# Kernel optimization log

Hardware: AMD Instinct MI355X
Metric: run time of the kernel (lower is better)

Reference implementation:

```python
import jax, jax.numpy as jnp
import numpy as np

SCALE = 64.0
MARGIN = 0.35
EPS = 1e-12  # torch F.normalize eps


def _l2norm(a, axis):
    n = jnp.sqrt(jnp.sum(a * a, axis=axis, keepdims=True))
    return a / jnp.maximum(n, EPS)


def setup_inputs() -> dict:
    key = jax.random.key(0)
    k1, k2, k3 = jax.random.split(key, 3)
    B, D, C = 512, 512, 100000
    x = jax.random.normal(k1, (B, D), dtype=jnp.float32)
    gt = jax.random.randint(k2, (B,), 0, C, dtype=jnp.int64)
    # kaiming_normal_ on [C, D]: std = sqrt(2 / fan_in) with fan_in = D
    wt = jax.random.normal(k3, (C, D), dtype=jnp.float32) * np.sqrt(2.0 / D)
    return {"x": x, "gt": gt, "wt": wt}


def reference(x, gt, wt):
    wt_norm = _l2norm(wt, axis=1)          # [C, D]
    x_norm = _l2norm(x, axis=1)            # [B, D]
    cos = jnp.einsum("bd,cd->bc", x_norm, wt_norm)  # [B, C]
    # margin only at target index (avoids materializing one-hot)
    b = jnp.arange(x.shape[0])
    margin_score = cos.at[b, gt].add(-MARGIN)
    logits = SCALE * margin_score
    logp = jax.nn.log_softmax(logits, axis=-1)
    nll = -logp[b, gt]
    return jnp.mean(nll)
```

## Files before the change

### kernel.cpp

```cpp
#include <hip/hip_runtime.h>
#include <hip/hip_bf16.h>

#define DIM 512
#define BATCH 512
#define CCLS 100000
#define BN 128
#define NT 782

typedef __attribute__((ext_vector_type(4))) float f32x4;

__device__ __forceinline__ void async_copy16(const unsigned char* g, unsigned char* l) {
  __builtin_amdgcn_global_load_lds((const __attribute__((address_space(1))) void*)g,
                                   (__attribute__((address_space(3))) void*)l, 16, 0, 0);
}

__global__ __launch_bounds__(256) void xquant(const float* __restrict__ x,
                                              unsigned char* __restrict__ xq,
                                              float* __restrict__ nx) {
  int wave = threadIdx.x >> 6;
  int lane = threadIdx.x & 63;
  int row = blockIdx.x * 4 + wave;
  const float4* src = (const float4*)(x + (size_t)row * DIM);
  float4 v0 = src[2 * lane];
  float4 v1 = src[2 * lane + 1];
  float ss = v0.x*v0.x + v0.y*v0.y + v0.z*v0.z + v0.w*v0.w
           + v1.x*v1.x + v1.y*v1.y + v1.z*v1.z + v1.w*v1.w;
  #pragma unroll
  for (int off = 32; off > 0; off >>= 1) ss += __shfl_xor(ss, off, 64);
  int p0 = __builtin_amdgcn_cvt_pk_fp8_f32(v0.x, v0.y, 0, false);
  p0     = __builtin_amdgcn_cvt_pk_fp8_f32(v0.z, v0.w, p0, true);
  int p1 = __builtin_amdgcn_cvt_pk_fp8_f32(v1.x, v1.y, 0, false);
  p1     = __builtin_amdgcn_cvt_pk_fp8_f32(v1.z, v1.w, p1, true);
  ((int2*)(xq + (size_t)row * DIM))[lane] = make_int2(p0, p1);
  if (lane == 0) nx[row] = fmaxf(sqrtf(ss), 1e-12f);
}

__global__ __launch_bounds__(1024) void cosface_fused(
    const unsigned char* __restrict__ xq,
    const float* __restrict__ wt,
    const int* __restrict__ gt,
    const float* __restrict__ nx,
    float* __restrict__ partial,
    float* __restrict__ tgt) {
  __shared__ __align__(16) unsigned char lds_a[512 * 128];
  __shared__ __align__(16) unsigned char lds_b[BN * 128];
  __shared__ float lds_rowsum[BATCH];
  __shared__ float lds_nx[BATCH];
  __shared__ float lds_nw[BN];
  __shared__ int lds_gt[BATCH];

  const int tid = threadIdx.x;
  const int lane = tid & 63;
  const int w = tid >> 6;
  const int wm = w >> 2;
  const int wn_ = w & 3;
  const int nt = blockIdx.x;

  if (tid < BATCH) {
    lds_rowsum[tid] = 0.f;
    lds_gt[tid] = gt[tid];
    lds_nx[tid] = nx[tid];
  }
  if (tid < BN) lds_nw[tid] = 0.f;

  unsigned int oa[4];
  #pragma unroll
  for (int j = 0; j < 4; ++j) {
    int c = j * 1024 + tid;
    int m = c >> 3;
    int qg = (c & 7) ^ (m & 7);
    oa[j] = (unsigned int)m * DIM + qg * 16;
  }
  const int mB = tid >> 3;
  const int qgB = (tid & 7) ^ (mB & 7);
  int rowB = nt * BN + mB;
  if (rowB >= CCLS) rowB = CCLS - 1;
  const float* wsrc = wt + (size_t)rowB * DIM + qgB * 16;

  f32x4 acc[8][2];
  #pragma unroll
  for (int i = 0; i < 8; ++i)
    #pragma unroll
    for (int j = 0; j < 2; ++j)
      acc[i][j] = (f32x4){0.f, 0.f, 0.f, 0.f};

  const int quad = lane >> 4;
  const int l15 = lane & 15;
  const int sw = l15 & 7;
  __syncthreads();

  for (int kk = 0; kk < 4; ++kk) {
    #pragma unroll
    for (int j = 0; j < 4; ++j)
      async_copy16(xq + oa[j] + kk * 128, &lds_a[(j * 1024 + w * 64) * 16]);
    {
      const float* p = wsrc + kk * 128;
      float4 f0 = *(const float4*)(p);
      float4 f1 = *(const float4*)(p + 4);
      float4 f2 = *(const float4*)(p + 8);
      float4 f3 = *(const float4*)(p + 12);
      f0.x*=16.f; f0.y*=16.f; f0.z*=16.f; f0.w*=16.f;
      f1.x*=16.f; f1.y*=16.f; f1.z*=16.f; f1.w*=16.f;
      f2.x*=16.f; f2.y*=16.f; f2.z*=16.f; f2.w*=16.f;
      f3.x*=16.f; f3.y*=16.f; f3.z*=16.f; f3.w*=16.f;
      float ss = f0.x*f0.x + f0.y*f0.y + f0.z*f0.z + f0.w*f0.w
               + f1.x*f1.x + f1.y*f1.y + f1.z*f1.z + f1.w*f1.w
               + f2.x*f2.x + f2.y*f2.y + f2.z*f2.z + f2.w*f2.w
               + f3.x*f3.x + f3.y*f3.y + f3.z*f3.z + f3.w*f3.w;
      int p0 = __builtin_amdgcn_cvt_pk_fp8_f32(f0.x, f0.y, 0, false);
      p0     = __builtin_amdgcn_cvt_pk_fp8_f32(f0.z, f0.w, p0, true);
      int p1 = __builtin_amdgcn_cvt_pk_fp8_f32(f1.x, f1.y, 0, false);
      p1     = __builtin_amdgcn_cvt_pk_fp8_f32(f1.z, f1.w, p1, true);
      int p2 = __builtin_amdgcn_cvt_pk_fp8_f32(f2.x, f2.y, 0, false);
      p2     = __builtin_amdgcn_cvt_pk_fp8_f32(f2.z, f2.w, p2, true);
      int p3 = __builtin_amdgcn_cvt_pk_fp8_f32(f3.x, f3.y, 0, false);
      p3     = __builtin_amdgcn_cvt_pk_fp8_f32(f3.z, f3.w, p3, true);
      ((int4*)lds_b)[tid] = make_int4(p0, p1, p2, p3);
      ss += __shfl_xor(ss, 1, 64);
      ss += __shfl_xor(ss, 2, 64);
      ss += __shfl_xor(ss, 4, 64);
      if ((lane & 7) == 0) atomicAdd(&lds_nw[mB], ss);
    }
    __syncthreads();

    #pragma unroll
    for (int s = 0; s < 4; ++s) {
      int g = s * 4 + quad;
      int cs = g >> 1;
      int h = (g & 1) * 8;
      long long af[8], bf[2];
      #pragma unroll
      for (int i = 0; i < 8; ++i)
        af[i] = *(const long long*)&lds_a[(wm * 128 + i * 16 + l15) * 128 + ((cs ^ sw) * 16) + h];
      #pragma unroll
      for (int j = 0; j < 2; ++j)
        bf[j] = *(const long long*)&lds_b[(wn_ * 32 + j * 16 + l15) * 128 + ((cs ^ sw) * 16) + h];
      #pragma unroll
      for (int i = 0; i < 8; ++i)
        #pragma unroll
        for (int j = 0; j < 2; ++j)
          acc[i][j] = __builtin_amdgcn_mfma_f32_16x16x32_fp8_fp8(af[i], bf[j], acc[i][j], 0, 0, 0);
    }
    __syncthreads();
  }

  float rnw[2];
  #pragma unroll
  for (int j = 0; j < 2; ++j)
    rnw[j] = 1.0f / fmaxf(sqrtf(lds_nw[wn_ * 32 + j * 16 + l15]), 1e-12f);
  #pragma unroll
  for (int i = 0; i < 8; ++i) {
    #pragma unroll
    for (int reg = 0; reg < 4; ++reg) {
      int m_loc = wm * 128 + i * 16 + quad * 4 + reg;
      int gtm = lds_gt[m_loc];
      float rx = 64.0f / lds_nx[m_loc];
      float s = 0.f;
      #pragma unroll
      for (int j = 0; j < 2; ++j) {
        int n_g = nt * BN + wn_ * 32 + j * 16 + l15;
        float logit = acc[i][j][reg] * rnw[j] * rx;
        if (n_g == gtm) {
          logit -= 64.f * 0.35f;
          tgt[m_loc] = logit;
        }
        if (n_g < CCLS) s += __expf(logit - 64.f);
      }
      #pragma unroll
      for (int off = 1; off < 16; off <<= 1) s += __shfl_xor(s, off, 64);
      if (l15 == 0) atomicAdd(&lds_rowsum[m_loc], s);
    }
  }
  __syncthreads();
  if (tid < BATCH)
    partial[(size_t)tid * NT + nt] = lds_rowsum[tid];
}

__global__ __launch_bounds__(64) void nll_rows(const float* __restrict__ partial,
                                               const float* __restrict__ tgt,
                                               float* __restrict__ nll) {
  int m = blockIdx.x;
  int lane = threadIdx.x;
  const float* row = partial + (size_t)m * NT;
  float s = 0.f;
  for (int t = lane; t < NT; t += 64) s += row[t];
  #pragma unroll
  for (int off = 32; off > 0; off >>= 1) s += __shfl_xor(s, off, 64);
  if (lane == 0) nll[m] = (logf(s) + 64.f) - tgt[m];
}

__global__ __launch_bounds__(512) void reduce_mean(const float* __restrict__ nll,
                                                   float* __restrict__ out) {
  __shared__ float red[BATCH];
  int m = threadIdx.x;
  red[m] = nll[m];
  __syncthreads();
  for (int k = 256; k > 0; k >>= 1) {
    if (m < k) red[m] += red[m + k];
    __syncthreads();
  }
  if (m == 0) out[0] = red[0] * (1.0f / BATCH);
}

extern "C" void kernel_launch(void* const* d_in, const int* in_sizes, int n_in,
                              void* d_out, int out_size, void* d_ws, size_t ws_size,
                              hipStream_t stream) {
  const float* x  = (const float*)d_in[0];
  const int*   gt = (const int*)d_in[1];
  const float* wt = (const float*)d_in[2];
  float* out = (float*)d_out;

  char* ws = (char*)d_ws;
  unsigned char* xq = (unsigned char*)ws;
  float* nx         = (float*)(ws + 262144);
  float* partial    = (float*)(ws + 264192);
  float* tgt        = (float*)(ws + 1865728);
  float* nll        = (float*)(ws + 1867776);

  xquant<<<BATCH / 4, 256, 0, stream>>>(x, xq, nx);
  cosface_fused<<<NT, 1024, 0, stream>>>(xq, wt, gt, nx, partial, tgt);
  nll_rows<<<BATCH, 64, 0, stream>>>(partial, tgt, nll);
  reduce_mean<<<1, BATCH, 0, stream>>>(nll, out);
}
```

Measured before the change: 393.7 us.

## Split GEMM tile into 256x64 blocks with XCD-aware mapping and weight prefetch

```diff
diff --git a/kernel.cpp b/kernel.cpp
--- a/kernel.cpp
+++ b/kernel.cpp
@@ -4,8 +4,9 @@
 #define DIM 512
 #define BATCH 512
 #define CCLS 100000
-#define BN 128
-#define NT 782
+#define BM 256
+#define BN 64
+#define NT 1563
 
 typedef __attribute__((ext_vector_type(4))) float f32x4;
 
@@ -35,41 +36,47 @@
   if (lane == 0) nx[row] = fmaxf(sqrtf(ss), 1e-12f);
 }
 
-__global__ __launch_bounds__(1024) void cosface_fused(
+__global__ __launch_bounds__(512, 4) void cosface_fused(
     const unsigned char* __restrict__ xq,
     const float* __restrict__ wt,
     const int* __restrict__ gt,
     const float* __restrict__ nx,
     float* __restrict__ partial,
     float* __restrict__ tgt) {
-  __shared__ __align__(16) unsigned char lds_a[512 * 128];
+  __shared__ __align__(16) unsigned char lds_a[BM * 128];
   __shared__ __align__(16) unsigned char lds_b[BN * 128];
-  __shared__ float lds_rowsum[BATCH];
-  __shared__ float lds_nx[BATCH];
+  __shared__ float lds_rowsum[BM];
+  __shared__ float lds_nx[BM];
   __shared__ float lds_nw[BN];
-  __shared__ int lds_gt[BATCH];
+  __shared__ int lds_gt[BM];
 
   const int tid = threadIdx.x;
   const int lane = tid & 63;
   const int w = tid >> 6;
-  const int wm = w >> 2;
-  const int wn_ = w & 3;
-  const int nt = blockIdx.x;
-
-  if (tid < BATCH) {
+  const int wm = w >> 1;
+  const int wn_ = w & 1;
+
+  int flat = blockIdx.x;
+  int xcd = flat & 7;
+  int idx = flat >> 3;
+  int f = ((xcd < 6) ? xcd * 391 : (6 * 391 + (xcd - 6) * 390)) + idx;
+  const int mt = f & 1;
+  const int nt = f >> 1;
+
+  if (tid < BM) {
     lds_rowsum[tid] = 0.f;
-    lds_gt[tid] = gt[tid];
-    lds_nx[tid] = nx[tid];
+    lds_gt[tid] = gt[mt * BM + tid];
+    lds_nx[tid] = nx[mt * BM + tid];
   }
   if (tid < BN) lds_nw[tid] = 0.f;
 
   unsigned int oa[4];
   #pragma unroll
   for (int j = 0; j < 4; ++j) {
-    int c = j * 1024 + tid;
+    int c = j * 512 + tid;
     int m = c >> 3;
     int qg = (c & 7) ^ (m & 7);
-    oa[j] = (unsigned int)m * DIM + qg * 16;
+    oa[j] = (unsigned int)(mt * BM + m) * DIM + qg * 16;
   }
   const int mB = tid >> 3;
   const int qgB = (tid & 7) ^ (mB & 7);
@@ -77,9 +84,9 @@
   if (rowB >= CCLS) rowB = CCLS - 1;
   const float* wsrc = wt + (size_t)rowB * DIM + qgB * 16;
 
-  f32x4 acc[8][2];
-  #pragma unroll
-  for (int i = 0; i < 8; ++i)
+  f32x4 acc[4][2];
+  #pragma unroll
+  for (int i = 0; i < 4; ++i)
     #pragma unroll
     for (int j = 0; j < 2; ++j)
       acc[i][j] = (f32x4){0.f, 0.f, 0.f, 0.f};
@@ -87,59 +94,91 @@
   const int quad = lane >> 4;
   const int l15 = lane & 15;
   const int sw = l15 & 7;
+
+  int p0, p1, p2, p3;
+  float ssq;
+  {
+    float4 f0 = *(const float4*)(wsrc);
+    float4 f1 = *(const float4*)(wsrc + 4);
+    float4 f2 = *(const float4*)(wsrc + 8);
+    float4 f3 = *(const float4*)(wsrc + 12);
+    f0.x*=16.f; f0.y*=16.f; f0.z*=16.f; f0.w*=16.f;
+    f1.x*=16.f; f1.y*=16.f; f1.z*=16.f; f1.w*=16.f;
+    f2.x*=16.f; f2.y*=16.f; f2.z*=16.f; f2.w*=16.f;
+    f3.x*=16.f; f3.y*=16.f; f3.z*=16.f; f3.w*=16.f;
+    ssq = f0.x*f0.x + f0.y*f0.y + f0.z*f0.z + f0.w*f0.w
+        + f1.x*f1.x + f1.y*f1.y + f1.z*f1.z + f1.w*f1.w
+        + f2.x*f2.x + f2.y*f2.y + f2.z*f2.z + f2.w*f2.w
+        + f3.x*f3.x + f3.y*f3.y + f3.z*f3.z + f3.w*f3.w;
+    p0 = __builtin_amdgcn_cvt_pk_fp8_f32(f0.x, f0.y, 0, false);
+    p0 = __builtin_amdgcn_cvt_pk_fp8_f32(f0.z, f0.w, p0, true);
+    p1 = __builtin_amdgcn_cvt_pk_fp8_f32(f1.x, f1.y, 0, false);
+    p1 = __builtin_amdgcn_cvt_pk_fp8_f32(f1.z, f1.w, p1, true);
+    p2 = __builtin_amdgcn_cvt_pk_fp8_f32(f2.x, f2.y, 0, false);
+    p2 = __builtin_amdgcn_cvt_pk_fp8_f32(f2.z, f2.w, p2, true);
+    p3 = __builtin_amdgcn_cvt_pk_fp8_f32(f3.x, f3.y, 0, false);
+    p3 = __builtin_amdgcn_cvt_pk_fp8_f32(f3.z, f3.w, p3, true);
+  }
   __syncthreads();
 
   for (int kk = 0; kk < 4; ++kk) {
+    ((int4*)lds_b)[tid] = make_int4(p0, p1, p2, p3);
     #pragma unroll
     for (int j = 0; j < 4; ++j)
-      async_copy16(xq + oa[j] + kk * 128, &lds_a[(j * 1024 + w * 64) * 16]);
+      async_copy16(xq + oa[j] + kk * 128, &lds_a[(j * 512 + w * 64) * 16]);
     {
-      const float* p = wsrc + kk * 128;
-      float4 f0 = *(const float4*)(p);
-      float4 f1 = *(const float4*)(p + 4);
-      float4 f2 = *(const float4*)(p + 8);
-      float4 f3 = *(const float4*)(p + 12);
+      float s = ssq;
+      s += __shfl_xor(s, 1, 64);
+      s += __shfl_xor(s, 2, 64);
+      s += __shfl_xor(s, 4, 64);
+      if ((lane & 7) == 0) atomicAdd(&lds_nw[mB], s);
+    }
+    __syncthreads();
+
+    float4 f0, f1, f2, f3;
+    if (kk < 3) {
+      const float* p = wsrc + (kk + 1) * 128;
+      f0 = *(const float4*)(p);
+      f1 = *(const float4*)(p + 4);
+      f2 = *(const float4*)(p + 8);
+      f3 = *(const float4*)(p + 12);
+    }
+    #pragma unroll
+    for (int s = 0; s < 4; ++s) {
+      int g = s * 4 + quad;
+      int cs = g >> 1;
+      int h = (g & 1) * 8;
+      long long af[4], bf[2];
+      #pragma unroll
+      for (int i = 0; i < 4; ++i)
+        af[i] = *(const long long*)&lds_a[(wm * 64 + i * 16 + l15) * 128 + ((cs ^ sw) * 16) + h];
+      #pragma unroll
+      for (int j = 0; j < 2; ++j)
+        bf[j] = *(const long long*)&lds_b[(wn_ * 32 + j * 16 + l15) * 128 + ((cs ^ sw) * 16) + h];
+      #pragma unroll
+      for (int i = 0; i < 4; ++i)
+        #pragma unroll
+        for (int j = 0; j < 2; ++j)
+          acc[i][j] = __builtin_amdgcn_mfma_f32_16x16x32_fp8_fp8(af[i], bf[j], acc[i][j], 0, 0, 0);
+    }
+
+    if (kk < 3) {
       f0.x*=16.f; f0.y*=16.f; f0.z*=16.f; f0.w*=16.f;
       f1.x*=16.f; f1.y*=16.f; f1.z*=16.f; f1.w*=16.f;
       f2.x*=16.f; f2.y*=16.f; f2.z*=16.f; f2.w*=16.f;
       f3.x*=16.f; f3.y*=16.f; f3.z*=16.f; f3.w*=16.f;
-      float ss = f0.x*f0.x + f0.y*f0.y + f0.z*f0.z + f0.w*f0.w
-               + f1.x*f1.x + f1.y*f1.y + f1.z*f1.z + f1.w*f1.w
-               + f2.x*f2.x + f2.y*f2.y + f2.z*f2.z + f2.w*f2.w
-               + f3.x*f3.x + f3.y*f3.y + f3.z*f3.z + f3.w*f3.w;
-      int p0 = __builtin_amdgcn_cvt_pk_fp8_f32(f0.x, f0.y, 0, false);
-      p0     = __builtin_amdgcn_cvt_pk_fp8_f32(f0.z, f0.w, p0, true);
-      int p1 = __builtin_amdgcn_cvt_pk_fp8_f32(f1.x, f1.y, 0, false);
-      p1     = __builtin_amdgcn_cvt_pk_fp8_f32(f1.z, f1.w, p1, true);
-      int p2 = __builtin_amdgcn_cvt_pk_fp8_f32(f2.x, f2.y, 0, false);
-      p2     = __builtin_amdgcn_cvt_pk_fp8_f32(f2.z, f2.w, p2, true);
-      int p3 = __builtin_amdgcn_cvt_pk_fp8_f32(f3.x, f3.y, 0, false);
-      p3     = __builtin_amdgcn_cvt_pk_fp8_f32(f3.z, f3.w, p3, true);
-      ((int4*)lds_b)[tid] = make_int4(p0, p1, p2, p3);
-      ss += __shfl_xor(ss, 1, 64);
-      ss += __shfl_xor(ss, 2, 64);
-      ss += __shfl_xor(ss, 4, 64);
-      if ((lane & 7) == 0) atomicAdd(&lds_nw[mB], ss);
-    }
-    __syncthreads();
-
-    #pragma unroll
-    for (int s = 0; s < 4; ++s) {
-      int g = s * 4 + quad;
-      int cs = g >> 1;
-      int h = (g & 1) * 8;
-      long long af[8], bf[2];
-      #pragma unroll
-      for (int i = 0; i < 8; ++i)
-        af[i] = *(const long long*)&lds_a[(wm * 128 + i * 16 + l15) * 128 + ((cs ^ sw) * 16) + h];
-      #pragma unroll
-      for (int j = 0; j < 2; ++j)
-        bf[j] = *(const long long*)&lds_b[(wn_ * 32 + j * 16 + l15) * 128 + ((cs ^ sw) * 16) + h];
-      #pragma unroll
-      for (int i = 0; i < 8; ++i)
-        #pragma unroll
-        for (int j = 0; j < 2; ++j)
-          acc[i][j] = __builtin_amdgcn_mfma_f32_16x16x32_fp8_fp8(af[i], bf[j], acc[i][j], 0, 0, 0);
+      ssq = f0.x*f0.x + f0.y*f0.y + f0.z*f0.z + f0.w*f0.w
+          + f1.x*f1.x + f1.y*f1.y + f1.z*f1.z + f1.w*f1.w
+          + f2.x*f2.x + f2.y*f2.y + f2.z*f2.z + f2.w*f2.w
+          + f3.x*f3.x + f3.y*f3.y + f3.z*f3.z + f3.w*f3.w;
+      p0 = __builtin_amdgcn_cvt_pk_fp8_f32(f0.x, f0.y, 0, false);
+      p0 = __builtin_amdgcn_cvt_pk_fp8_f32(f0.z, f0.w, p0, true);
+      p1 = __builtin_amdgcn_cvt_pk_fp8_f32(f1.x, f1.y, 0, false);
+      p1 = __builtin_amdgcn_cvt_pk_fp8_f32(f1.z, f1.w, p1, true);
+      p2 = __builtin_amdgcn_cvt_pk_fp8_f32(f2.x, f2.y, 0, false);
+      p2 = __builtin_amdgcn_cvt_pk_fp8_f32(f2.z, f2.w, p2, true);
+      p3 = __builtin_amdgcn_cvt_pk_fp8_f32(f3.x, f3.y, 0, false);
+      p3 = __builtin_amdgcn_cvt_pk_fp8_f32(f3.z, f3.w, p3, true);
     }
     __syncthreads();
   }
@@ -149,10 +188,10 @@
   for (int j = 0; j < 2; ++j)
     rnw[j] = 1.0f / fmaxf(sqrtf(lds_nw[wn_ * 32 + j * 16 + l15]), 1e-12f);
   #pragma unroll
-  for (int i = 0; i < 8; ++i) {
+  for (int i = 0; i < 4; ++i) {
     #pragma unroll
     for (int reg = 0; reg < 4; ++reg) {
-      int m_loc = wm * 128 + i * 16 + quad * 4 + reg;
+      int m_loc = wm * 64 + i * 16 + quad * 4 + reg;
       int gtm = lds_gt[m_loc];
       float rx = 64.0f / lds_nx[m_loc];
       float s = 0.f;
@@ -162,7 +201,7 @@
         float logit = acc[i][j][reg] * rnw[j] * rx;
         if (n_g == gtm) {
           logit -= 64.f * 0.35f;
-          tgt[m_loc] = logit;
+          tgt[mt * BM + m_loc] = logit;
         }
         if (n_g < CCLS) s += __expf(logit - 64.f);
       }
@@ -172,8 +211,8 @@
     }
   }
   __syncthreads();
-  if (tid < BATCH)
-    partial[(size_t)tid * NT + nt] = lds_rowsum[tid];
+  if (tid < BM)
+    partial[(size_t)(mt * BM + tid) * NT + nt] = lds_rowsum[tid];
 }
 
 __global__ __launch_bounds__(64) void nll_rows(const float* __restrict__ partial,
@@ -214,11 +253,11 @@
   unsigned char* xq = (unsigned char*)ws;
   float* nx         = (float*)(ws + 262144);
   float* partial    = (float*)(ws + 264192);
-  float* tgt        = (float*)(ws + 1865728);
-  float* nll        = (float*)(ws + 1867776);
+  float* tgt        = (float*)(ws + 3465216);
+  float* nll        = (float*)(ws + 3467264);
 
   xquant<<<BATCH / 4, 256, 0, stream>>>(x, xq, nx);
-  cosface_fused<<<NT, 1024, 0, stream>>>(xq, wt, gt, nx, partial, tgt);
+  cosface_fused<<<2 * NT, 512, 0, stream>>>(xq, wt, gt, nx, partial, tgt);
   nll_rows<<<BATCH, 64, 0, stream>>>(partial, tgt, nll);
   reduce_mean<<<1, BATCH, 0, stream>>>(nll, out);
 }
```

Measured after the change: 348.5 us. 1.13x faster.

## Split batch into 128-row tiles, double-buffer weight tiles, and swizzle block order

Applied to the files above, without the earlier changes.

```diff
diff --git a/kernel.cpp b/kernel.cpp
--- a/kernel.cpp
+++ b/kernel.cpp
@@ -4,6 +4,7 @@
 #define DIM 512
 #define BATCH 512
 #define CCLS 100000
+#define BM 128
 #define BN 128
 #define NT 782
 
@@ -35,51 +36,86 @@
   if (lane == 0) nx[row] = fmaxf(sqrtf(ss), 1e-12f);
 }
 
-__global__ __launch_bounds__(1024) void cosface_fused(
+__global__ __launch_bounds__(512, 2) void cosface_fused(
     const unsigned char* __restrict__ xq,
     const float* __restrict__ wt,
     const int* __restrict__ gt,
     const float* __restrict__ nx,
     float* __restrict__ partial,
     float* __restrict__ tgt) {
-  __shared__ __align__(16) unsigned char lds_a[512 * 128];
-  __shared__ __align__(16) unsigned char lds_b[BN * 128];
-  __shared__ float lds_rowsum[BATCH];
-  __shared__ float lds_nx[BATCH];
+  __shared__ __align__(16) unsigned char lds_a[BM * DIM];
+  __shared__ __align__(16) unsigned char lds_b[2][BN * 128];
+  __shared__ float lds_rowsum[BM];
+  __shared__ float lds_nx[BM];
   __shared__ float lds_nw[BN];
-  __shared__ int lds_gt[BATCH];
+  __shared__ int lds_gt[BM];
 
   const int tid = threadIdx.x;
   const int lane = tid & 63;
   const int w = tid >> 6;
   const int wm = w >> 2;
   const int wn_ = w & 3;
-  const int nt = blockIdx.x;
-
-  if (tid < BATCH) {
+
+  int flat = blockIdx.x;
+  int f = (flat & 7) * 391 + (flat >> 3);
+  const int mt = f & 3;
+  const int nt = f >> 2;
+
+  if (tid < BM) {
     lds_rowsum[tid] = 0.f;
-    lds_gt[tid] = gt[tid];
-    lds_nx[tid] = nx[tid];
-  }
-  if (tid < BN) lds_nw[tid] = 0.f;
-
-  unsigned int oa[4];
-  #pragma unroll
-  for (int j = 0; j < 4; ++j) {
-    int c = j * 1024 + tid;
-    int m = c >> 3;
-    int qg = (c & 7) ^ (m & 7);
-    oa[j] = (unsigned int)m * DIM + qg * 16;
-  }
-  const int mB = tid >> 3;
-  const int qgB = (tid & 7) ^ (mB & 7);
-  int rowB = nt * BN + mB;
-  if (rowB >= CCLS) rowB = CCLS - 1;
-  const float* wsrc = wt + (size_t)rowB * DIM + qgB * 16;
-
-  f32x4 acc[8][2];
-  #pragma unroll
-  for (int i = 0; i < 8; ++i)
+    lds_gt[tid] = gt[mt * BM + tid];
+    lds_nx[tid] = nx[mt * BM + tid];
+  }
+
+  #pragma unroll
+  for (int j = 0; j < 8; ++j) {
+    int c = j * 512 + tid;
+    int m = c >> 5;
+    int qs = c & 31;
+    int src = (mt * BM + m) * DIM + (((qs & 24) | ((qs & 7) ^ (m & 7))) << 4);
+    async_copy16(xq + src, &lds_a[(j * 512 + w * 64) * 16]);
+  }
+
+  const int r0 = tid >> 3;
+  const int r1 = r0 + 64;
+  const int qg = (tid & 7) ^ (r0 & 7);
+  int rowB0 = nt * BN + r0; if (rowB0 >= CCLS) rowB0 = CCLS - 1;
+  int rowB1 = nt * BN + r1; if (rowB1 >= CCLS) rowB1 = CCLS - 1;
+  const float* wsrc0 = wt + (size_t)rowB0 * DIM + qg * 16;
+  const float* wsrc1 = wt + (size_t)rowB1 * DIM + qg * 16;
+
+#define LOADB(K) do {                                                        \
+    const float* pa_ = wsrc0 + (K) * 128;                                    \
+    a0 = *(const float4*)(pa_);     a1 = *(const float4*)(pa_ + 4);          \
+    a2 = *(const float4*)(pa_ + 8); a3 = *(const float4*)(pa_ + 12);         \
+    const float* pb_ = wsrc1 + (K) * 128;                                    \
+    b0 = *(const float4*)(pb_);     b1 = *(const float4*)(pb_ + 4);          \
+    b2 = *(const float4*)(pb_ + 8); b3 = *(const float4*)(pb_ + 12);         \
+  } while (0)
+
+#define QUANT16(P, SS, F0, F1, F2, F3) do {                                  \
+    F0.x*=16.f; F0.y*=16.f; F0.z*=16.f; F0.w*=16.f;                          \
+    F1.x*=16.f; F1.y*=16.f; F1.z*=16.f; F1.w*=16.f;                          \
+    F2.x*=16.f; F2.y*=16.f; F2.z*=16.f; F2.w*=16.f;                          \
+    F3.x*=16.f; F3.y*=16.f; F3.z*=16.f; F3.w*=16.f;                          \
+    SS += F0.x*F0.x + F0.y*F0.y + F0.z*F0.z + F0.w*F0.w                      \
+        + F1.x*F1.x + F1.y*F1.y + F1.z*F1.z + F1.w*F1.w                      \
+        + F2.x*F2.x + F2.y*F2.y + F2.z*F2.z + F2.w*F2.w                      \
+        + F3.x*F3.x + F3.y*F3.y + F3.z*F3.z + F3.w*F3.w;                     \
+    int q0_ = __builtin_amdgcn_cvt_pk_fp8_f32(F0.x, F0.y, 0, false);         \
+    q0_     = __builtin_amdgcn_cvt_pk_fp8_f32(F0.z, F0.w, q0_, true);        \
+    int q1_ = __builtin_amdgcn_cvt_pk_fp8_f32(F1.x, F1.y, 0, false);         \
+    q1_     = __builtin_amdgcn_cvt_pk_fp8_f32(F1.z, F1.w, q1_, true);        \
+    int q2_ = __builtin_amdgcn_cvt_pk_fp8_f32(F2.x, F2.y, 0, false);         \
+    q2_     = __builtin_amdgcn_cvt_pk_fp8_f32(F2.z, F2.w, q2_, true);        \
+    int q3_ = __builtin_amdgcn_cvt_pk_fp8_f32(F3.x, F3.y, 0, false);         \
+    q3_     = __builtin_amdgcn_cvt_pk_fp8_f32(F3.z, F3.w, q3_, true);        \
+    P = make_int4(q0_, q1_, q2_, q3_);                                       \
+  } while (0)
+
+  f32x4 acc[4][2];
+  #pragma unroll
+  for (int i = 0; i < 4; ++i)
     #pragma unroll
     for (int j = 0; j < 2; ++j)
       acc[i][j] = (f32x4){0.f, 0.f, 0.f, 0.f};
@@ -87,72 +123,74 @@
   const int quad = lane >> 4;
   const int l15 = lane & 15;
   const int sw = l15 & 7;
-  __syncthreads();
-
+  float4 a0, a1, a2, a3, b0, b1, b2, b3;
+  int4 pA, pB;
+  float ss0 = 0.f, ss1 = 0.f;
+
+  LOADB(0);
+  QUANT16(pA, ss0, a0, a1, a2, a3);
+  QUANT16(pB, ss1, b0, b1, b2, b3);
+  ((int4*)lds_b[0])[tid] = pA;
+  ((int4*)lds_b[0])[512 + tid] = pB;
+  LOADB(1);
+  QUANT16(pA, ss0, a0, a1, a2, a3);
+  QUANT16(pB, ss1, b0, b1, b2, b3);
+  __syncthreads();
+
+  #pragma unroll
   for (int kk = 0; kk < 4; ++kk) {
-    #pragma unroll
-    for (int j = 0; j < 4; ++j)
-      async_copy16(xq + oa[j] + kk * 128, &lds_a[(j * 1024 + w * 64) * 16]);
-    {
-      const float* p = wsrc + kk * 128;
-      float4 f0 = *(const float4*)(p);
-      float4 f1 = *(const float4*)(p + 4);
-      float4 f2 = *(const float4*)(p + 8);
-      float4 f3 = *(const float4*)(p + 12);
-      f0.x*=16.f; f0.y*=16.f; f0.z*=16.f; f0.w*=16.f;
-      f1.x*=16.f; f1.y*=16.f; f1.z*=16.f; f1.w*=16.f;
-      f2.x*=16.f; f2.y*=16.f; f2.z*=16.f; f2.w*=16.f;
-      f3.x*=16.f; f3.y*=16.f; f3.z*=16.f; f3.w*=16.f;
-      float ss = f0.x*f0.x + f0.y*f0.y + f0.z*f0.z + f0.w*f0.w
-               + f1.x*f1.x + f1.y*f1.y + f1.z*f1.z + f1.w*f1.w
-               + f2.x*f2.x + f2.y*f2.y + f2.z*f2.z + f2.w*f2.w
-               + f3.x*f3.x + f3.y*f3.y + f3.z*f3.z + f3.w*f3.w;
-      int p0 = __builtin_amdgcn_cvt_pk_fp8_f32(f0.x, f0.y, 0, false);
-      p0     = __builtin_amdgcn_cvt_pk_fp8_f32(f0.z, f0.w, p0, true);
-      int p1 = __builtin_amdgcn_cvt_pk_fp8_f32(f1.x, f1.y, 0, false);
-      p1     = __builtin_amdgcn_cvt_pk_fp8_f32(f1.z, f1.w, p1, true);
-      int p2 = __builtin_amdgcn_cvt_pk_fp8_f32(f2.x, f2.y, 0, false);
-      p2     = __builtin_amdgcn_cvt_pk_fp8_f32(f2.z, f2.w, p2, true);
-      int p3 = __builtin_amdgcn_cvt_pk_fp8_f32(f3.x, f3.y, 0, false);
-      p3     = __builtin_amdgcn_cvt_pk_fp8_f32(f3.z, f3.w, p3, true);
-      ((int4*)lds_b)[tid] = make_int4(p0, p1, p2, p3);
-      ss += __shfl_xor(ss, 1, 64);
-      ss += __shfl_xor(ss, 2, 64);
-      ss += __shfl_xor(ss, 4, 64);
-      if ((lane & 7) == 0) atomicAdd(&lds_nw[mB], ss);
-    }
-    __syncthreads();
+    if (kk < 3) {
+      ((int4*)lds_b[(kk + 1) & 1])[tid] = pA;
+      ((int4*)lds_b[(kk + 1) & 1])[512 + tid] = pB;
+    }
+    if (kk < 2) LOADB(kk + 2);
 
     #pragma unroll
     for (int s = 0; s < 4; ++s) {
       int g = s * 4 + quad;
       int cs = g >> 1;
       int h = (g & 1) * 8;
-      long long af[8], bf[2];
-      #pragma unroll
-      for (int i = 0; i < 8; ++i)
-        af[i] = *(const long long*)&lds_a[(wm * 128 + i * 16 + l15) * 128 + ((cs ^ sw) * 16) + h];
+      long long af[4], bf[2];
+      #pragma unroll
+      for (int i = 0; i < 4; ++i)
+        af[i] = *(const long long*)&lds_a[(wm * 64 + i * 16 + l15) * DIM + kk * 128 + ((cs ^ sw) * 16) + h];
       #pragma unroll
       for (int j = 0; j < 2; ++j)
-        bf[j] = *(const long long*)&lds_b[(wn_ * 32 + j * 16 + l15) * 128 + ((cs ^ sw) * 16) + h];
-      #pragma unroll
-      for (int i = 0; i < 8; ++i)
+        bf[j] = *(const long long*)&lds_b[kk & 1][(wn_ * 32 + j * 16 + l15) * 128 + ((cs ^ sw) * 16) + h];
+      #pragma unroll
+      for (int i = 0; i < 4; ++i)
         #pragma unroll
         for (int j = 0; j < 2; ++j)
           acc[i][j] = __builtin_amdgcn_mfma_f32_16x16x32_fp8_fp8(af[i], bf[j], acc[i][j], 0, 0, 0);
     }
-    __syncthreads();
-  }
+
+    if (kk < 2) {
+      QUANT16(pA, ss0, a0, a1, a2, a3);
+      QUANT16(pB, ss1, b0, b1, b2, b3);
+    }
+    if (kk < 3) __syncthreads();
+  }
+#undef LOADB
+#undef QUANT16
+
+  ss0 += __shfl_xor(ss0, 1, 64); ss1 += __shfl_xor(ss1, 1, 64);
+  ss0 += __shfl_xor(ss0, 2, 64); ss1 += __shfl_xor(ss1, 2, 64);
+  ss0 += __shfl_xor(ss0, 4, 64); ss1 += __shfl_xor(ss1, 4, 64);
+  if ((lane & 7) == 0) {
+    lds_nw[r0] = ss0;
+    lds_nw[r1] = ss1;
+  }
+  __syncthreads();
 
   float rnw[2];
   #pragma unroll
   for (int j = 0; j < 2; ++j)
     rnw[j] = 1.0f / fmaxf(sqrtf(lds_nw[wn_ * 32 + j * 16 + l15]), 1e-12f);
   #pragma unroll
-  for (int i = 0; i < 8; ++i) {
+  for (int i = 0; i < 4; ++i) {
     #pragma unroll
     for (int reg = 0; reg < 4; ++reg) {
-      int m_loc = wm * 128 + i * 16 + quad * 4 + reg;
+      int m_loc = wm * 64 + i * 16 + quad * 4 + reg;
       int gtm = lds_gt[m_loc];
       float rx = 64.0f / lds_nx[m_loc];
       float s = 0.f;
@@ -162,7 +200,7 @@
         float logit = acc[i][j][reg] * rnw[j] * rx;
         if (n_g == gtm) {
           logit -= 64.f * 0.35f;
-          tgt[m_loc] = logit;
+          tgt[mt * BM + m_loc] = logit;
         }
         if (n_g < CCLS) s += __expf(logit - 64.f);
       }
@@ -172,8 +210,8 @@
     }
   }
   __syncthreads();
-  if (tid < BATCH)
-    partial[(size_t)tid * NT + nt] = lds_rowsum[tid];
+  if (tid < BM)
+    partial[(size_t)(mt * BM + tid) * NT + nt] = lds_rowsum[tid];
 }
 
 __global__ __launch_bounds__(64) void nll_rows(const float* __restrict__ partial,
@@ -218,7 +256,7 @@
   float* nll        = (float*)(ws + 1867776);
 
   xquant<<<BATCH / 4, 256, 0, stream>>>(x, xq, nx);
-  cosface_fused<<<NT, 1024, 0, stream>>>(xq, wt, gt, nx, partial, tgt);
+  cosface_fused<<<4 * NT, 512, 0, stream>>>(xq, wt, gt, nx, partial, tgt);
   nll_rows<<<BATCH, 64, 0, stream>>>(partial, tgt, nll);
   reduce_mean<<<1, BATCH, 0, stream>>>(nll, out);
 }
```

Result: slower. 435.8 us (+10.7%).

## Halve class tile and double-buffer LDS with software-pipelined W quantization

Applied to the files above, without the earlier changes.

```diff
diff --git a/kernel.cpp b/kernel.cpp
--- a/kernel.cpp
+++ b/kernel.cpp
@@ -4,8 +4,9 @@
 #define DIM 512
 #define BATCH 512
 #define CCLS 100000
-#define BN 128
-#define NT 782
+#define BM 512
+#define BN 64
+#define NT 1563
 
 typedef __attribute__((ext_vector_type(4))) float f32x4;
 
@@ -35,33 +36,32 @@
   if (lane == 0) nx[row] = fmaxf(sqrtf(ss), 1e-12f);
 }
 
-__global__ __launch_bounds__(1024) void cosface_fused(
+__global__ __launch_bounds__(1024, 4) void cosface_fused(
     const unsigned char* __restrict__ xq,
     const float* __restrict__ wt,
     const int* __restrict__ gt,
     const float* __restrict__ nx,
     float* __restrict__ partial,
     float* __restrict__ tgt) {
-  __shared__ __align__(16) unsigned char lds_a[512 * 128];
-  __shared__ __align__(16) unsigned char lds_b[BN * 128];
-  __shared__ float lds_rowsum[BATCH];
-  __shared__ float lds_nx[BATCH];
+  __shared__ __align__(16) unsigned char lds_a[2][BM * 128];
+  __shared__ __align__(16) unsigned char lds_b[2][BN * 128];
+  __shared__ float lds_rowsum[BM];
+  __shared__ float lds_nx[BM];
   __shared__ float lds_nw[BN];
-  __shared__ int lds_gt[BATCH];
+  __shared__ int lds_gt[BM];
 
   const int tid = threadIdx.x;
   const int lane = tid & 63;
   const int w = tid >> 6;
-  const int wm = w >> 2;
-  const int wn_ = w & 3;
+  const int wm = w >> 1;
+  const int wn_ = w & 1;
   const int nt = blockIdx.x;
 
-  if (tid < BATCH) {
+  if (tid < BM) {
     lds_rowsum[tid] = 0.f;
     lds_gt[tid] = gt[tid];
     lds_nx[tid] = nx[tid];
   }
-  if (tid < BN) lds_nw[tid] = 0.f;
 
   unsigned int oa[4];
   #pragma unroll
@@ -71,15 +71,48 @@
     int qg = (c & 7) ^ (m & 7);
     oa[j] = (unsigned int)m * DIM + qg * 16;
   }
-  const int mB = tid >> 3;
-  const int qgB = (tid & 7) ^ (mB & 7);
-  int rowB = nt * BN + mB;
+#define STAGEA(sel, kk) do {                                                 \
+    _Pragma("unroll")                                                        \
+    for (int j = 0; j < 4; ++j)                                              \
+      async_copy16(xq + oa[j] + (kk) * 128,                                  \
+                   &lds_a[sel][(j * 1024 + w * 64) * 16]);                   \
+  } while (0)
+
+  const int r0 = tid >> 3;
+  const int qg = (tid & 7) ^ (r0 & 7);
+  int rowB = nt * BN + r0;
   if (rowB >= CCLS) rowB = CCLS - 1;
-  const float* wsrc = wt + (size_t)rowB * DIM + qgB * 16;
-
-  f32x4 acc[8][2];
-  #pragma unroll
-  for (int i = 0; i < 8; ++i)
+  const float* wsrc = wt + (size_t)rowB * DIM + qg * 16;
+
+#define LOADB(K) do {                                                        \
+    const float* p_ = wsrc + (K) * 128;                                      \
+    a0 = *(const float4*)(p_);     a1 = *(const float4*)(p_ + 4);            \
+    a2 = *(const float4*)(p_ + 8); a3 = *(const float4*)(p_ + 12);           \
+  } while (0)
+
+#define QUANT16() do {                                                       \
+    a0.x*=16.f; a0.y*=16.f; a0.z*=16.f; a0.w*=16.f;                          \
+    a1.x*=16.f; a1.y*=16.f; a1.z*=16.f; a1.w*=16.f;                          \
+    a2.x*=16.f; a2.y*=16.f; a2.z*=16.f; a2.w*=16.f;                          \
+    a3.x*=16.f; a3.y*=16.f; a3.z*=16.f; a3.w*=16.f;                          \
+    ss0 += a0.x*a0.x + a0.y*a0.y + a0.z*a0.z + a0.w*a0.w                     \
+         + a1.x*a1.x + a1.y*a1.y + a1.z*a1.z + a1.w*a1.w                     \
+         + a2.x*a2.x + a2.y*a2.y + a2.z*a2.z + a2.w*a2.w                     \
+         + a3.x*a3.x + a3.y*a3.y + a3.z*a3.z + a3.w*a3.w;                    \
+    int q0_ = __builtin_amdgcn_cvt_pk_fp8_f32(a0.x, a0.y, 0, false);         \
+    q0_     = __builtin_amdgcn_cvt_pk_fp8_f32(a0.z, a0.w, q0_, true);        \
+    int q1_ = __builtin_amdgcn_cvt_pk_fp8_f32(a1.x, a1.y, 0, false);         \
+    q1_     = __builtin_amdgcn_cvt_pk_fp8_f32(a1.z, a1.w, q1_, true);        \
+    int q2_ = __builtin_amdgcn_cvt_pk_fp8_f32(a2.x, a2.y, 0, false);         \
+    q2_     = __builtin_amdgcn_cvt_pk_fp8_f32(a2.z, a2.w, q2_, true);        \
+    int q3_ = __builtin_amdgcn_cvt_pk_fp8_f32(a3.x, a3.y, 0, false);         \
+    q3_     = __builtin_amdgcn_cvt_pk_fp8_f32(a3.z, a3.w, q3_, true);        \
+    pA = make_int4(q0_, q1_, q2_, q3_);                                      \
+  } while (0)
+
+  f32x4 acc[4][2];
+  #pragma unroll
+  for (int i = 0; i < 4; ++i)
     #pragma unroll
     for (int j = 0; j < 2; ++j)
       acc[i][j] = (f32x4){0.f, 0.f, 0.f, 0.f};
@@ -87,72 +120,73 @@
   const int quad = lane >> 4;
   const int l15 = lane & 15;
   const int sw = l15 & 7;
-  __syncthreads();
-
+  float4 a0, a1, a2, a3;
+  int4 pA;
+  float ss0 = 0.f;
+  const bool bown = (tid < 512);
+
+  STAGEA(0, 0);
+  if (bown) {
+    LOADB(0);
+    QUANT16();
+    ((int4*)lds_b[0])[tid] = pA;
+    LOADB(1);
+    QUANT16();
+  }
+  __syncthreads();
+
+  #pragma unroll
   for (int kk = 0; kk < 4; ++kk) {
-    #pragma unroll
-    for (int j = 0; j < 4; ++j)
-      async_copy16(xq + oa[j] + kk * 128, &lds_a[(j * 1024 + w * 64) * 16]);
-    {
-      const float* p = wsrc + kk * 128;
-      float4 f0 = *(const float4*)(p);
-      float4 f1 = *(const float4*)(p + 4);
-      float4 f2 = *(const float4*)(p + 8);
-      float4 f3 = *(const float4*)(p + 12);
-      f0.x*=16.f; f0.y*=16.f; f0.z*=16.f; f0.w*=16.f;
-      f1.x*=16.f; f1.y*=16.f; f1.z*=16.f; f1.w*=16.f;
-      f2.x*=16.f; f2.y*=16.f; f2.z*=16.f; f2.w*=16.f;
-      f3.x*=16.f; f3.y*=16.f; f3.z*=16.f; f3.w*=16.f;
-      float ss = f0.x*f0.x + f0.y*f0.y + f0.z*f0.z + f0.w*f0.w
-               + f1.x*f1.x + f1.y*f1.y + f1.z*f1.z + f1.w*f1.w
-               + f2.x*f2.x + f2.y*f2.y + f2.z*f2.z + f2.w*f2.w
-               + f3.x*f3.x + f3.y*f3.y + f3.z*f3.z + f3.w*f3.w;
-      int p0 = __builtin_amdgcn_cvt_pk_fp8_f32(f0.x, f0.y, 0, false);
-      p0     = __builtin_amdgcn_cvt_pk_fp8_f32(f0.z, f0.w, p0, true);
-      int p1 = __builtin_amdgcn_cvt_pk_fp8_f32(f1.x, f1.y, 0, false);
-      p1     = __builtin_amdgcn_cvt_pk_fp8_f32(f1.z, f1.w, p1, true);
-      int p2 = __builtin_amdgcn_cvt_pk_fp8_f32(f2.x, f2.y, 0, false);
-      p2     = __builtin_amdgcn_cvt_pk_fp8_f32(f2.z, f2.w, p2, true);
-      int p3 = __builtin_amdgcn_cvt_pk_fp8_f32(f3.x, f3.y, 0, false);
-      p3     = __builtin_amdgcn_cvt_pk_fp8_f32(f3.z, f3.w, p3, true);
-      ((int4*)lds_b)[tid] = make_int4(p0, p1, p2, p3);
-      ss += __shfl_xor(ss, 1, 64);
-      ss += __shfl_xor(ss, 2, 64);
-      ss += __shfl_xor(ss, 4, 64);
-      if ((lane & 7) == 0) atomicAdd(&lds_nw[mB], ss);
+    const int cur = kk & 1;
+    if (kk < 3 && bown) {
+      ((int4*)lds_b[cur ^ 1])[tid] = pA;
     }
-    __syncthreads();
+    if (kk < 3) STAGEA(cur ^ 1, kk + 1);
+    if (kk < 2 && bown) LOADB(kk + 2);
 
     #pragma unroll
     for (int s = 0; s < 4; ++s) {
       int g = s * 4 + quad;
       int cs = g >> 1;
       int h = (g & 1) * 8;
-      long long af[8], bf[2];
-      #pragma unroll
-      for (int i = 0; i < 8; ++i)
-        af[i] = *(const long long*)&lds_a[(wm * 128 + i * 16 + l15) * 128 + ((cs ^ sw) * 16) + h];
+      long long af[4], bf[2];
+      #pragma unroll
+      for (int i = 0; i < 4; ++i)
+        af[i] = *(const long long*)&lds_a[cur][(wm * 64 + i * 16 + l15) * 128 + ((cs ^ sw) * 16) + h];
       #pragma unroll
       for (int j = 0; j < 2; ++j)
-        bf[j] = *(const long long*)&lds_b[(wn_ * 32 + j * 16 + l15) * 128 + ((cs ^ sw) * 16) + h];
-      #pragma unroll
-      for (int i = 0; i < 8; ++i)
+        bf[j] = *(const long long*)&lds_b[cur][(wn_ * 32 + j * 16 + l15) * 128 + ((cs ^ sw) * 16) + h];
+      #pragma unroll
+      for (int i = 0; i < 4; ++i)
         #pragma unroll
         for (int j = 0; j < 2; ++j)
           acc[i][j] = __builtin_amdgcn_mfma_f32_16x16x32_fp8_fp8(af[i], bf[j], acc[i][j], 0, 0, 0);
     }
-    __syncthreads();
-  }
+
+    if (kk < 2 && bown) QUANT16();
+    if (kk < 3) __syncthreads();
+  }
+#undef STAGEA
+#undef LOADB
+#undef QUANT16
+
+  if (bown) {
+    ss0 += __shfl_xor(ss0, 1, 64);
+    ss0 += __shfl_xor(ss0, 2, 64);
+    ss0 += __shfl_xor(ss0, 4, 64);
+    if ((lane & 7) == 0) lds_nw[r0] = ss0;
+  }
+  __syncthreads();
 
   float rnw[2];
   #pragma unroll
   for (int j = 0; j < 2; ++j)
     rnw[j] = 1.0f / fmaxf(sqrtf(lds_nw[wn_ * 32 + j * 16 + l15]), 1e-12f);
   #pragma unroll
-  for (int i = 0; i < 8; ++i) {
+  for (int i = 0; i < 4; ++i) {
     #pragma unroll
     for (int reg = 0; reg < 4; ++reg) {
-      int m_loc = wm * 128 + i * 16 + quad * 4 + reg;
+      int m_loc = wm * 64 + i * 16 + quad * 4 + reg;
       int gtm = lds_gt[m_loc];
       float rx = 64.0f / lds_nx[m_loc];
       float s = 0.f;
@@ -172,7 +206,7 @@
     }
   }
   __syncthreads();
-  if (tid < BATCH)
+  if (tid < BM)
     partial[(size_t)tid * NT + nt] = lds_rowsum[tid];
 }
 
@@ -214,8 +248,8 @@
   unsigned char* xq = (unsigned char*)ws;
   float* nx         = (float*)(ws + 262144);
   float* partial    = (float*)(ws + 264192);
-  float* tgt        = (float*)(ws + 1865728);
-  float* nll        = (float*)(ws + 1867776);
+  float* tgt        = (float*)(ws + 3465216);
+  float* nll        = (float*)(ws + 3467264);
 
   xquant<<<BATCH / 4, 256, 0, stream>>>(x, xq, nx);
   cosface_fused<<<NT, 1024, 0, stream>>>(xq, wt, gt, nx, partial, tgt);
```

Measured after the change: 364.2 us. 7.5% less time.
